# Kernel tuning notes

Measured on AMD Instinct MI355X. Metric: run time of the kernel, lower is better.

The kernel has to match this reference:

```python
import jax, jax.numpy as jnp
import numpy as np

N_NODES = 50000
N_EDGES = 640000
DIM_IN = 128
DIM_OUT = 128
NUM_GRAPHS = 64


def setup_inputs() -> dict:
    key = jax.random.key(0)
    ks = jax.random.split(key, 8)
    x = jax.random.normal(ks[0], (N_NODES, DIM_IN), dtype=jnp.float32)
    edge_index = jax.random.randint(ks[1], (2, N_EDGES), 0, N_NODES, dtype=jnp.int32)
    batch = jnp.sort(jax.random.randint(ks[2], (N_NODES,), 0, NUM_GRAPHS, dtype=jnp.int32))
    s = 1.0 / np.sqrt(DIM_IN)
    W1 = jax.random.normal(ks[3], (DIM_IN, DIM_IN), dtype=jnp.float32) * s
    W2 = jax.random.normal(ks[4], (DIM_IN, DIM_IN), dtype=jnp.float32) * s
    Wlin = jax.random.normal(ks[5], (DIM_IN, DIM_OUT), dtype=jnp.float32) * s
    b1 = jnp.zeros((DIM_IN,), jnp.float32)
    b2 = jnp.zeros((DIM_IN,), jnp.float32)
    blin = jnp.zeros((DIM_OUT,), jnp.float32)
    return {"x": x, "edge_index": edge_index, "batch": batch,
            "W1": W1, "b1": b1, "W2": W2, "b2": b2, "Wlin": Wlin, "blin": blin}


def _gcn_conv(x, W, b, src, dst, n_nodes):
    # GCNConv: symmetric norm with self-loops: D^{-1/2}(A+I)D^{-1/2} X W + b
    h = x @ W                                                   # [N, d]
    deg = jax.ops.segment_sum(jnp.ones_like(dst, jnp.float32), dst,
                              num_segments=n_nodes) + 1.0       # +1 self loop
    dinv = jax.lax.rsqrt(deg)                                   # [N]
    w = dinv[src] * dinv[dst]                                   # per-edge norm [E]
    agg = jax.ops.segment_sum(h[src] * w[:, None], dst, num_segments=n_nodes)
    return agg + h * (dinv * dinv)[:, None] + b                 # self-loop term + bias


def reference(x, edge_index, batch, W1, b1, W2, b2, Wlin, blin):
    n = x.shape[0]
    src, dst = edge_index[0], edge_index[1]
    h = jax.nn.relu(_gcn_conv(x, W1, b1, src, dst, n))          # dropout = identity (eval)
    h = _gcn_conv(h, W2, b2, src, dst, n)
    # global mean pool over graphs
    s = jax.ops.segment_sum(h, batch, num_segments=NUM_GRAPHS)  # [G, d]
    cnt = jax.ops.segment_sum(jnp.ones((n,), jnp.float32), batch, num_segments=NUM_GRAPHS)
    pooled = s / jnp.maximum(cnt, 1.0)[:, None]
    return jax.nn.relu(pooled @ Wlin + blin)
```

## Files before the change

kernel.cpp:

```cpp
#include <hip/hip_runtime.h>

#define N_NODES   50000
#define N_EDGES   640000
#define DIM       128
#define NUM_GRAPHS 64
#define SLOTS     64
#define GEMM1_BLOCKS 196
#define FILL_BLOCKS  313

typedef __attribute__((ext_vector_type(8))) short          s16x8;
typedef __attribute__((ext_vector_type(8))) unsigned short u16x8;
typedef __attribute__((ext_vector_type(4))) float          f32x4;

__device__ inline float bf2f(unsigned short u) {
    unsigned v = ((unsigned)u) << 16;
    float f;
    __builtin_memcpy(&f, &v, 4);
    return f;
}
__device__ inline unsigned short f2bf(float f) {
    unsigned u;
    __builtin_memcpy(&u, &f, 4);
    u = (u + 0x7fffu + ((u >> 16) & 1u)) >> 16;
    return (unsigned short)u;
}

__global__ __launch_bounds__(128) void k_prep_w(const float* __restrict__ W1,
                                                const float* __restrict__ W2,
                                                unsigned short* __restrict__ Wt1,
                                                unsigned short* __restrict__ Wt2,
                                                int* __restrict__ cnt,
                                                float* __restrict__ pooled) {
    int k = blockIdx.x & 127;
    const float*    W  = (blockIdx.x < DIM) ? W1 : W2;
    unsigned short* Wt = (blockIdx.x < DIM) ? Wt1 : Wt2;
    int n = threadIdx.x;
    Wt[n * DIM + k] = f2bf(W[k * DIM + n]);

    int gid = blockIdx.x * 128 + threadIdx.x;
    for (int i = gid; i < N_NODES; i += 32768) cnt[i] = 0;
    if (gid < NUM_GRAPHS * DIM) pooled[gid] = 0.f;
}

__global__ __launch_bounds__(512) void k_fill_gemm1(const int* __restrict__ src,
                                                    const int* __restrict__ dst,
                                                    int* __restrict__ cnt,
                                                    unsigned short* __restrict__ slots,
                                                    const float* __restrict__ x,
                                                    const unsigned short* __restrict__ Wt1,
                                                    unsigned short* __restrict__ H1) {
    __shared__ unsigned short wsh[DIM][136];
    const int tid = threadIdx.x;

    if (blockIdx.x >= GEMM1_BLOCKS) {
        int e0 = ((blockIdx.x - GEMM1_BLOCKS) * 512 + tid) * 4;
        if (e0 >= N_EDGES) return;
        int4 s4 = *reinterpret_cast<const int4*>(src + e0);
        int4 d4 = *reinterpret_cast<const int4*>(dst + e0);
        int p0 = atomicAdd(&cnt[d4.x], 1);
        int p1 = atomicAdd(&cnt[d4.y], 1);
        int p2 = atomicAdd(&cnt[d4.z], 1);
        int p3 = atomicAdd(&cnt[d4.w], 1);
        if (p0 < SLOTS) slots[d4.x * SLOTS + p0] = (unsigned short)s4.x;
        if (p1 < SLOTS) slots[d4.y * SLOTS + p1] = (unsigned short)s4.y;
        if (p2 < SLOTS) slots[d4.z * SLOTS + p2] = (unsigned short)s4.z;
        if (p3 < SLOTS) slots[d4.w * SLOTS + p3] = (unsigned short)s4.w;
        return;
    }

    #pragma unroll
    for (int i = 0; i < 4; i++) {
        int off = tid * 8 + i * 4096;
        int r = off >> 7, cc = off & 127;
        u16x8 v = *reinterpret_cast<const u16x8*>(Wt1 + off);
        *reinterpret_cast<u16x8*>(&wsh[r][cc]) = v;
    }
    __syncthreads();

    const int wid  = tid >> 6;
    const int lane = tid & 63;
    const int l15  = lane & 15;
    const int lk   = lane >> 4;
    const int row0 = blockIdx.x * 256 + wid * 32;

    f32x4 acc[2][8];
    #pragma unroll
    for (int a = 0; a < 2; a++)
        #pragma unroll
        for (int n = 0; n < 8; n++) acc[a][n] = (f32x4){0.f, 0.f, 0.f, 0.f};

    const long long r0 = min(row0 + l15,      N_NODES - 1);
    const long long r1 = min(row0 + 16 + l15, N_NODES - 1);

    #pragma unroll
    for (int kk = 0; kk < 4; kk++) {
        const int kb = kk * 32 + lk * 8;
        s16x8 a0, a1;
        const float4 p0 = *reinterpret_cast<const float4*>(x + r0 * DIM + kb);
        const float4 q0 = *reinterpret_cast<const float4*>(x + r0 * DIM + kb + 4);
        const float4 p1 = *reinterpret_cast<const float4*>(x + r1 * DIM + kb);
        const float4 q1 = *reinterpret_cast<const float4*>(x + r1 * DIM + kb + 4);
        a0[0]=(short)f2bf(p0.x); a0[1]=(short)f2bf(p0.y); a0[2]=(short)f2bf(p0.z); a0[3]=(short)f2bf(p0.w);
        a0[4]=(short)f2bf(q0.x); a0[5]=(short)f2bf(q0.y); a0[6]=(short)f2bf(q0.z); a0[7]=(short)f2bf(q0.w);
        a1[0]=(short)f2bf(p1.x); a1[1]=(short)f2bf(p1.y); a1[2]=(short)f2bf(p1.z); a1[3]=(short)f2bf(p1.w);
        a1[4]=(short)f2bf(q1.x); a1[5]=(short)f2bf(q1.y); a1[6]=(short)f2bf(q1.z); a1[7]=(short)f2bf(q1.w);
        #pragma unroll
        for (int n = 0; n < 8; n++) {
            s16x8 b = *reinterpret_cast<const s16x8*>(&wsh[n * 16 + l15][kb]);
            acc[0][n] = __builtin_amdgcn_mfma_f32_16x16x32_bf16(a0, b, acc[0][n], 0, 0, 0);
            acc[1][n] = __builtin_amdgcn_mfma_f32_16x16x32_bf16(a1, b, acc[1][n], 0, 0, 0);
        }
    }

    #pragma unroll
    for (int rh = 0; rh < 2; rh++) {
        #pragma unroll
        for (int j = 0; j < 4; j++) {
            int row = row0 + rh * 16 + lk * 4 + j;
            if (row < N_NODES) {
                #pragma unroll
                for (int n = 0; n < 8; n++)
                    H1[(long long)row * DIM + n * 16 + l15] = f2bf(acc[rh][n][j]);
            }
        }
    }
}

__device__ inline void gather_node(const int* __restrict__ cnt,
                                   const unsigned short* __restrict__ slots,
                                   const unsigned short* __restrict__ h,
                                   const float* __restrict__ bias,
                                   int n, int c, float dn, float* acc) {
    float d2 = dn * dn;
    u16x8 hv = *reinterpret_cast<const u16x8*>(h + (size_t)n * DIM + c);
    #pragma unroll
    for (int j = 0; j < 8; j++) acc[j] = bf2f(hv[j]) * d2 + bias[c + j];

    const int m = min(cnt[n], SLOTS);
    const unsigned short* sl = slots + (size_t)n * SLOTS;

    int i = 0;
    for (; i + 3 < m; i += 4) {
        int s0 = sl[i], s1 = sl[i + 1], s2 = sl[i + 2], s3 = sl[i + 3];
        float w0 = rsqrtf((float)cnt[s0] + 1.0f) * dn;
        float w1 = rsqrtf((float)cnt[s1] + 1.0f) * dn;
        float w2 = rsqrtf((float)cnt[s2] + 1.0f) * dn;
        float w3 = rsqrtf((float)cnt[s3] + 1.0f) * dn;
        u16x8 v0 = *reinterpret_cast<const u16x8*>(h + (size_t)s0 * DIM + c);
        u16x8 v1 = *reinterpret_cast<const u16x8*>(h + (size_t)s1 * DIM + c);
        u16x8 v2 = *reinterpret_cast<const u16x8*>(h + (size_t)s2 * DIM + c);
        u16x8 v3 = *reinterpret_cast<const u16x8*>(h + (size_t)s3 * DIM + c);
        #pragma unroll
        for (int j = 0; j < 8; j++)
            acc[j] += (bf2f(v0[j]) * w0 + bf2f(v1[j]) * w1) +
                      (bf2f(v2[j]) * w2 + bf2f(v3[j]) * w3);
    }
    for (; i < m; i++) {
        int s0 = sl[i];
        float w0 = rsqrtf((float)cnt[s0] + 1.0f) * dn;
        u16x8 v0 = *reinterpret_cast<const u16x8*>(h + (size_t)s0 * DIM + c);
        #pragma unroll
        for (int j = 0; j < 8; j++) acc[j] += bf2f(v0[j]) * w0;
    }
}

__global__ __launch_bounds__(512) void k_pull1g(const int* __restrict__ cnt,
                                                const unsigned short* __restrict__ slots,
                                                const unsigned short* __restrict__ h,
                                                const float* __restrict__ bias,
                                                const unsigned short* __restrict__ Wt2,
                                                unsigned short* __restrict__ H2) {
    __shared__ unsigned short zl[32][136];
    const int tid  = threadIdx.x;
    const int base = blockIdx.x * 32;
    const int ln   = tid >> 4;
    const int n    = base + ln;
    const int c    = (tid & 15) << 3;

    u16x8 o = (u16x8){0, 0, 0, 0, 0, 0, 0, 0};
    if (n < N_NODES) {
        float dn = rsqrtf((float)cnt[n] + 1.0f);
        float acc[8];
        gather_node(cnt, slots, h, bias, n, c, dn, acc);
        #pragma unroll
        for (int j = 0; j < 8; j++) o[j] = f2bf(fmaxf(acc[j], 0.f));
    }
    *reinterpret_cast<u16x8*>(&zl[ln][c]) = o;
    __syncthreads();

    const int wid = tid >> 6;
    const int lane = tid & 63;
    const int l15 = lane & 15;
    const int lk  = lane >> 4;
    const int rh  = wid >> 2;
    const int cp  = (wid & 3) * 2;

    f32x4 accm[2];
    accm[0] = (f32x4){0.f, 0.f, 0.f, 0.f};
    accm[1] = (f32x4){0.f, 0.f, 0.f, 0.f};

    #pragma unroll
    for (int kk = 0; kk < 4; kk++) {
        const int kb = kk * 32 + lk * 8;
        s16x8 a = *reinterpret_cast<const s16x8*>(&zl[rh * 16 + l15][kb]);
        #pragma unroll
        for (int t2 = 0; t2 < 2; t2++) {
            s16x8 b = *reinterpret_cast<const s16x8*>(Wt2 + (size_t)((cp + t2) * 16 + l15) * DIM + kb);
            accm[t2] = __builtin_amdgcn_mfma_f32_16x16x32_bf16(a, b, accm[t2], 0, 0, 0);
        }
    }

    #pragma unroll
    for (int t2 = 0; t2 < 2; t2++) {
        const int col = (cp + t2) * 16 + l15;
        #pragma unroll
        for (int j = 0; j < 4; j++) {
            int row = base + rh * 16 + lk * 4 + j;
            if (row < N_NODES)
                H2[(size_t)row * DIM + col] = f2bf(accm[t2][j]);
        }
    }
}

__global__ __launch_bounds__(256) void k_pull_pool(const int* __restrict__ cnt,
                                                   const unsigned short* __restrict__ slots,
                                                   const unsigned short* __restrict__ h,
                                                   const float* __restrict__ bias,
                                                   const int* __restrict__ batch,
                                                   float* __restrict__ pooled) {
    __shared__ float pool_l[2][DIM];
    const int tid  = threadIdx.x;
    const int base = blockIdx.x * 16;
    const int n    = base + (tid >> 4);
    const int c    = (tid & 15) << 3;

    pool_l[tid >> 7][tid & 127] = 0.f;
    __syncthreads();

    float dn = rsqrtf((float)cnt[n] + 1.0f);
    float acc[8];
    gather_node(cnt, slots, h, bias, n, c, dn, acc);

    const int g    = batch[n];
    const int gmin = batch[base];
    const int d    = g - gmin;

    if (__all(g == __shfl(g, 0))) {
        #pragma unroll
        for (int j = 0; j < 8; j++) {
            acc[j] += __shfl_xor(acc[j], 16);
            acc[j] += __shfl_xor(acc[j], 32);
        }
        if ((tid & 63) < 16) {
            if (d < 2) {
                #pragma unroll
                for (int j = 0; j < 8; j++) atomicAdd(&pool_l[d][c + j], acc[j]);
            } else {
                #pragma unroll
                for (int j = 0; j < 8; j++) atomicAdd(&pooled[g * DIM + c + j], acc[j]);
            }
        }
    } else {
        if (d < 2) {
            #pragma unroll
            for (int j = 0; j < 8; j++) atomicAdd(&pool_l[d][c + j], acc[j]);
        } else {
            #pragma unroll
            for (int j = 0; j < 8; j++) atomicAdd(&pooled[g * DIM + c + j], acc[j]);
        }
    }
    __syncthreads();

    const int f = tid & 127;
    if (tid < 128) {
        atomicAdd(&pooled[gmin * DIM + f], pool_l[0][f]);
    } else {
        int gmax = batch[base + 15];
        if (gmax > gmin) atomicAdd(&pooled[(gmin + 1) * DIM + f], pool_l[1][f]);
    }
}

__global__ __launch_bounds__(128) void k_pool2(const float* __restrict__ pooled,
                                               const int* __restrict__ batch,
                                               const float* __restrict__ Wlin,
                                               const float* __restrict__ blin,
                                               float* __restrict__ out) {
    int g = blockIdx.x;
    int t = threadIdx.x;
    __shared__ int se[2];
    __shared__ float pr[DIM];
    if (t < 2) {
        int target = g + t;
        int lo = 0, hi = N_NODES;
        while (lo < hi) { int mid = (lo + hi) >> 1; if (batch[mid] < target) lo = mid + 1; else hi = mid; }
        se[t] = lo;
    }
    __syncthreads();
    float inv_cnt = 1.0f / fmaxf((float)(se[1] - se[0]), 1.0f);
    pr[t] = pooled[g * DIM + t] * inv_cnt;
    __syncthreads();
    float acc = blin[t];
    #pragma unroll 8
    for (int k = 0; k < DIM; k++) acc += pr[k] * Wlin[k * DIM + t];
    out[g * DIM + t] = fmaxf(acc, 0.f);
}

extern "C" void kernel_launch(void* const* d_in, const int* in_sizes, int n_in,
                              void* d_out, int out_size, void* d_ws, size_t ws_size,
                              hipStream_t stream) {
    const float* x          = (const float*)d_in[0];
    const int*   edge_index = (const int*)d_in[1];
    const int*   batch      = (const int*)d_in[2];
    const float* W1         = (const float*)d_in[3];
    const float* b1         = (const float*)d_in[4];
    const float* W2         = (const float*)d_in[5];
    const float* b2         = (const float*)d_in[6];
    const float* Wlin       = (const float*)d_in[7];
    const float* blin       = (const float*)d_in[8];
    float*       out        = (float*)d_out;

    const int* src = edge_index;
    const int* dst = edge_index + N_EDGES;

    char* ws = (char*)d_ws;
    size_t off = 0;
    auto alloc = [&](size_t bytes) { void* p = ws + off; off = (off + bytes + 255) & ~255ULL; return p; };
    int*            cnt    = (int*)            alloc((size_t)N_NODES * 4);
    unsigned short* slots  = (unsigned short*) alloc((size_t)N_NODES * SLOTS * 2);
    float*          pooled = (float*)          alloc((size_t)NUM_GRAPHS * DIM * 4);
    unsigned short* Wt1    = (unsigned short*) alloc((size_t)DIM * DIM * 2);
    unsigned short* Wt2    = (unsigned short*) alloc((size_t)DIM * DIM * 2);
    unsigned short* H1     = (unsigned short*) alloc((size_t)N_NODES * DIM * 2);
    unsigned short* H2     = (unsigned short*) alloc((size_t)N_NODES * DIM * 2);

    const int pull1Blocks = (N_NODES + 31) / 32;
    const int pullBlocks  = (N_NODES * 16 + 255) / 256;

    k_prep_w<<<2 * DIM, DIM, 0, stream>>>(W1, W2, Wt1, Wt2, cnt, pooled);

    k_fill_gemm1<<<GEMM1_BLOCKS + FILL_BLOCKS, 512, 0, stream>>>(src, dst, cnt, slots, x, Wt1, H1);

    k_pull1g<<<pull1Blocks, 512, 0, stream>>>(cnt, slots, H1, b1, Wt2, H2);

    k_pull_pool<<<pullBlocks, 256, 0, stream>>>(cnt, slots, H2, b2, batch, pooled);

    k_pool2<<<NUM_GRAPHS, 128, 0, stream>>>(pooled, batch, Wlin, blin, out);
}
```

Before: 126.2 us.

## Split pull1 from GEMM2 and gather each node with a full wave

The fused gather+GEMM kernel is split into a standalone aggregation kernel that writes Z1 and a separate MFMA GEMM kernel that stages W2 in shared memory. Both gather kernels now give each node a full 64-lane wave, with four lanes per column chunk each taking every fourth neighbor and combining through shuffles. This raises memory-level parallelism for the irregular neighbor gathers. The cost is an extra kernel launch and an extra N×128 bf16 round trip through global memory for Z1.

```diff
diff --git a/kernel.cpp b/kernel.cpp
--- a/kernel.cpp
+++ b/kernel.cpp
@@ -126,103 +126,130 @@
     }
 }
 
-__device__ inline void gather_node(const int* __restrict__ cnt,
+__global__ __launch_bounds__(512) void k_gemm2(const unsigned short* __restrict__ Ab,
+                                               const unsigned short* __restrict__ Wt,
+                                               unsigned short* __restrict__ H) {
+    __shared__ unsigned short wsh[DIM][136];
+    const int tid = threadIdx.x;
+
+    #pragma unroll
+    for (int i = 0; i < 4; i++) {
+        int off = tid * 8 + i * 4096;
+        int r = off >> 7, cc = off & 127;
+        u16x8 v = *reinterpret_cast<const u16x8*>(Wt + off);
+        *reinterpret_cast<u16x8*>(&wsh[r][cc]) = v;
+    }
+    __syncthreads();
+
+    const int wid  = tid >> 6;
+    const int lane = tid & 63;
+    const int l15  = lane & 15;
+    const int lk   = lane >> 4;
+    const int row0 = blockIdx.x * 256 + wid * 32;
+
+    f32x4 acc[2][8];
+    #pragma unroll
+    for (int a = 0; a < 2; a++)
+        #pragma unroll
+        for (int n = 0; n < 8; n++) acc[a][n] = (f32x4){0.f, 0.f, 0.f, 0.f};
+
+    const long long r0 = min(row0 + l15,      N_NODES - 1);
+    const long long r1 = min(row0 + 16 + l15, N_NODES - 1);
+
+    #pragma unroll
+    for (int kk = 0; kk < 4; kk++) {
+        const int kb = kk * 32 + lk * 8;
+        s16x8 a0 = *reinterpret_cast<const s16x8*>(Ab + r0 * DIM + kb);
+        s16x8 a1 = *reinterpret_cast<const s16x8*>(Ab + r1 * DIM + kb);
+        #pragma unroll
+        for (int n = 0; n < 8; n++) {
+            s16x8 b = *reinterpret_cast<const s16x8*>(&wsh[n * 16 + l15][kb]);
+            acc[0][n] = __builtin_amdgcn_mfma_f32_16x16x32_bf16(a0, b, acc[0][n], 0, 0, 0);
+            acc[1][n] = __builtin_amdgcn_mfma_f32_16x16x32_bf16(a1, b, acc[1][n], 0, 0, 0);
+        }
+    }
+
+    #pragma unroll
+    for (int rh = 0; rh < 2; rh++) {
+        #pragma unroll
+        for (int j = 0; j < 4; j++) {
+            int row = row0 + rh * 16 + lk * 4 + j;
+            if (row < N_NODES) {
+                #pragma unroll
+                for (int n = 0; n < 8; n++)
+                    H[(long long)row * DIM + n * 16 + l15] = f2bf(acc[rh][n][j]);
+            }
+        }
+    }
+}
+
+__device__ inline void gather_wave(const int* __restrict__ cnt,
                                    const unsigned short* __restrict__ slots,
                                    const unsigned short* __restrict__ h,
                                    const float* __restrict__ bias,
-                                   int n, int c, float dn, float* acc) {
-    float d2 = dn * dn;
-    u16x8 hv = *reinterpret_cast<const u16x8*>(h + (size_t)n * DIM + c);
-    #pragma unroll
-    for (int j = 0; j < 8; j++) acc[j] = bf2f(hv[j]) * d2 + bias[c + j];
+                                   int n, int c, int way, float dn, float* acc) {
+    if (way == 0) {
+        float d2 = dn * dn;
+        u16x8 hv = *reinterpret_cast<const u16x8*>(h + (size_t)n * DIM + c);
+        #pragma unroll
+        for (int j = 0; j < 8; j++) acc[j] = bf2f(hv[j]) * d2 + bias[c + j];
+    } else {
+        #pragma unroll
+        for (int j = 0; j < 8; j++) acc[j] = 0.f;
+    }
 
     const int m = min(cnt[n], SLOTS);
     const unsigned short* sl = slots + (size_t)n * SLOTS;
 
-    int i = 0;
-    for (; i + 3 < m; i += 4) {
-        int s0 = sl[i], s1 = sl[i + 1], s2 = sl[i + 2], s3 = sl[i + 3];
+    int i = way;
+    for (; i + 4 < m; i += 8) {
+        int s0 = sl[i], s1 = sl[i + 4];
         float w0 = rsqrtf((float)cnt[s0] + 1.0f) * dn;
         float w1 = rsqrtf((float)cnt[s1] + 1.0f) * dn;
-        float w2 = rsqrtf((float)cnt[s2] + 1.0f) * dn;
-        float w3 = rsqrtf((float)cnt[s3] + 1.0f) * dn;
         u16x8 v0 = *reinterpret_cast<const u16x8*>(h + (size_t)s0 * DIM + c);
         u16x8 v1 = *reinterpret_cast<const u16x8*>(h + (size_t)s1 * DIM + c);
-        u16x8 v2 = *reinterpret_cast<const u16x8*>(h + (size_t)s2 * DIM + c);
-        u16x8 v3 = *reinterpret_cast<const u16x8*>(h + (size_t)s3 * DIM + c);
-        #pragma unroll
-        for (int j = 0; j < 8; j++)
-            acc[j] += (bf2f(v0[j]) * w0 + bf2f(v1[j]) * w1) +
-                      (bf2f(v2[j]) * w2 + bf2f(v3[j]) * w3);
-    }
-    for (; i < m; i++) {
+        #pragma unroll
+        for (int j = 0; j < 8; j++) acc[j] += bf2f(v0[j]) * w0 + bf2f(v1[j]) * w1;
+    }
+    if (i < m) {
         int s0 = sl[i];
         float w0 = rsqrtf((float)cnt[s0] + 1.0f) * dn;
         u16x8 v0 = *reinterpret_cast<const u16x8*>(h + (size_t)s0 * DIM + c);
         #pragma unroll
         for (int j = 0; j < 8; j++) acc[j] += bf2f(v0[j]) * w0;
     }
-}
-
-__global__ __launch_bounds__(512) void k_pull1g(const int* __restrict__ cnt,
-                                                const unsigned short* __restrict__ slots,
-                                                const unsigned short* __restrict__ h,
-                                                const float* __restrict__ bias,
-                                                const unsigned short* __restrict__ Wt2,
-                                                unsigned short* __restrict__ H2) {
-    __shared__ unsigned short zl[32][136];
+
+    #pragma unroll
+    for (int j = 0; j < 8; j++) {
+        acc[j] += __shfl_xor(acc[j], 16);
+        acc[j] += __shfl_xor(acc[j], 32);
+    }
+}
+
+__global__ __launch_bounds__(512) void k_pull1(const int* __restrict__ cnt,
+                                               const unsigned short* __restrict__ slots,
+                                               const unsigned short* __restrict__ h,
+                                               const float* __restrict__ bias,
+                                               unsigned short* __restrict__ outp) {
     const int tid  = threadIdx.x;
-    const int base = blockIdx.x * 32;
-    const int ln   = tid >> 4;
-    const int n    = base + ln;
-    const int c    = (tid & 15) << 3;
-
-    u16x8 o = (u16x8){0, 0, 0, 0, 0, 0, 0, 0};
-    if (n < N_NODES) {
-        float dn = rsqrtf((float)cnt[n] + 1.0f);
-        float acc[8];
-        gather_node(cnt, slots, h, bias, n, c, dn, acc);
+    const int n    = blockIdx.x * 8 + (tid >> 6);
+    const int lane = tid & 63;
+    const int way  = lane >> 4;
+    const int c    = (lane & 15) << 3;
+
+    float dn = rsqrtf((float)cnt[n] + 1.0f);
+    float acc[8];
+    gather_wave(cnt, slots, h, bias, n, c, way, dn, acc);
+
+    if (way == 0) {
+        u16x8 o;
         #pragma unroll
         for (int j = 0; j < 8; j++) o[j] = f2bf(fmaxf(acc[j], 0.f));
-    }
-    *reinterpret_cast<u16x8*>(&zl[ln][c]) = o;
-    __syncthreads();
-
-    const int wid = tid >> 6;
-    const int lane = tid & 63;
-    const int l15 = lane & 15;
-    const int lk  = lane >> 4;
-    const int rh  = wid >> 2;
-    const int cp  = (wid & 3) * 2;
-
-    f32x4 accm[2];
-    accm[0] = (f32x4){0.f, 0.f, 0.f, 0.f};
-    accm[1] = (f32x4){0.f, 0.f, 0.f, 0.f};
-
-    #pragma unroll
-    for (int kk = 0; kk < 4; kk++) {
-        const int kb = kk * 32 + lk * 8;
-        s16x8 a = *reinterpret_cast<const s16x8*>(&zl[rh * 16 + l15][kb]);
-        #pragma unroll
-        for (int t2 = 0; t2 < 2; t2++) {
-            s16x8 b = *reinterpret_cast<const s16x8*>(Wt2 + (size_t)((cp + t2) * 16 + l15) * DIM + kb);
-            accm[t2] = __builtin_amdgcn_mfma_f32_16x16x32_bf16(a, b, accm[t2], 0, 0, 0);
-        }
-    }
-
-    #pragma unroll
-    for (int t2 = 0; t2 < 2; t2++) {
-        const int col = (cp + t2) * 16 + l15;
-        #pragma unroll
-        for (int j = 0; j < 4; j++) {
-            int row = base + rh * 16 + lk * 4 + j;
-            if (row < N_NODES)
-                H2[(size_t)row * DIM + col] = f2bf(accm[t2][j]);
-        }
-    }
-}
-
-__global__ __launch_bounds__(256) void k_pull_pool(const int* __restrict__ cnt,
+        *reinterpret_cast<u16x8*>(outp + (size_t)n * DIM + c) = o;
+    }
+}
+
+__global__ __launch_bounds__(512) void k_pull_pool(const int* __restrict__ cnt,
                                                    const unsigned short* __restrict__ slots,
                                                    const unsigned short* __restrict__ h,
                                                    const float* __restrict__ bias,
@@ -230,37 +257,24 @@
                                                    float* __restrict__ pooled) {
     __shared__ float pool_l[2][DIM];
     const int tid  = threadIdx.x;
-    const int base = blockIdx.x * 16;
-    const int n    = base + (tid >> 4);
-    const int c    = (tid & 15) << 3;
-
-    pool_l[tid >> 7][tid & 127] = 0.f;
+    const int base = blockIdx.x * 8;
+    const int n    = base + (tid >> 6);
+    const int lane = tid & 63;
+    const int way  = lane >> 4;
+    const int c    = (lane & 15) << 3;
+
+    if (tid < 256) pool_l[tid >> 7][tid & 127] = 0.f;
     __syncthreads();
 
     float dn = rsqrtf((float)cnt[n] + 1.0f);
     float acc[8];
-    gather_node(cnt, slots, h, bias, n, c, dn, acc);
+    gather_wave(cnt, slots, h, bias, n, c, way, dn, acc);
 
     const int g    = batch[n];
     const int gmin = batch[base];
     const int d    = g - gmin;
 
-    if (__all(g == __shfl(g, 0))) {
-        #pragma unroll
-        for (int j = 0; j < 8; j++) {
-            acc[j] += __shfl_xor(acc[j], 16);
-            acc[j] += __shfl_xor(acc[j], 32);
-        }
-        if ((tid & 63) < 16) {
-            if (d < 2) {
-                #pragma unroll
-                for (int j = 0; j < 8; j++) atomicAdd(&pool_l[d][c + j], acc[j]);
-            } else {
-                #pragma unroll
-                for (int j = 0; j < 8; j++) atomicAdd(&pooled[g * DIM + c + j], acc[j]);
-            }
-        }
-    } else {
+    if (way == 0) {
         if (d < 2) {
             #pragma unroll
             for (int j = 0; j < 8; j++) atomicAdd(&pool_l[d][c + j], acc[j]);
@@ -274,8 +288,8 @@
     const int f = tid & 127;
     if (tid < 128) {
         atomicAdd(&pooled[gmin * DIM + f], pool_l[0][f]);
-    } else {
-        int gmax = batch[base + 15];
+    } else if (tid < 256) {
+        int gmax = batch[base + 7];
         if (gmax > gmin) atomicAdd(&pooled[(gmin + 1) * DIM + f], pool_l[1][f]);
     }
 }
@@ -331,18 +345,21 @@
     unsigned short* Wt1    = (unsigned short*) alloc((size_t)DIM * DIM * 2);
     unsigned short* Wt2    = (unsigned short*) alloc((size_t)DIM * DIM * 2);
     unsigned short* H1     = (unsigned short*) alloc((size_t)N_NODES * DIM * 2);
+    unsigned short* Z1     = (unsigned short*) alloc((size_t)N_NODES * DIM * 2);
     unsigned short* H2     = (unsigned short*) alloc((size_t)N_NODES * DIM * 2);
 
-    const int pull1Blocks = (N_NODES + 31) / 32;
-    const int pullBlocks  = (N_NODES * 16 + 255) / 256;
+    const int pullBlocks = N_NODES / 8;
+    const int gemmBlocks = (N_NODES + 255) / 256;
 
     k_prep_w<<<2 * DIM, DIM, 0, stream>>>(W1, W2, Wt1, Wt2, cnt, pooled);
 
     k_fill_gemm1<<<GEMM1_BLOCKS + FILL_BLOCKS, 512, 0, stream>>>(src, dst, cnt, slots, x, Wt1, H1);
 
-    k_pull1g<<<pull1Blocks, 512, 0, stream>>>(cnt, slots, H1, b1, Wt2, H2);
-
-    k_pull_pool<<<pullBlocks, 256, 0, stream>>>(cnt, slots, H2, b2, batch, pooled);
+    k_pull1<<<pullBlocks, 512, 0, stream>>>(cnt, slots, H1, b1, Z1);
+
+    k_gemm2<<<gemmBlocks, 512, 0, stream>>>(Z1, Wt2, H2);
+
+    k_pull_pool<<<pullBlocks, 512, 0, stream>>>(cnt, slots, H2, b2, batch, pooled);
 
     k_pool2<<<NUM_GRAPHS, 128, 0, stream>>>(pooled, batch, Wlin, blin, out);
 }
```

Result: slower. 143.6 us (+13.7%).
